# Performance work log

Measured on AMD Instinct MI355X. Metric: run time of the kernel, lower is better.

## Reference

```python
import jax, jax.numpy as jnp
import numpy as np

DILATIONS = (1, 2, 4, 8, 16, 32, 64, 128, 256, 512)
K = 3            # kernel_size
CH = 128         # channels
B, T = 4, 16384
L = len(DILATIONS)


def _conv1x1(x, w, b=None):
    # x: [B, Cin, T], w: [Cout, Cin, 1] -> [B, Cout, T]
    y = jnp.einsum('oc,bct->bot', w[..., 0], x)
    return y if b is None else y + b[None, :, None]


def _causal_dilated_conv(x, w, b, d):
    # buffer of zeros of size (K-1)*d concatenated on the left == causal left pad
    pad = (K - 1) * d
    y = jax.lax.conv_general_dilated(
        x, w, window_strides=(1,), padding=[(pad, 0)], rhs_dilation=(d,),
        dimension_numbers=('NCH', 'OIH', 'NCH'))
    return y + b[None, :, None]


def setup_inputs() -> dict:
    key = jax.random.key(0)
    ks = jax.random.split(key, 12)
    s = 0.1  # keep gated activations out of saturation
    return {
        'x': jax.random.normal(ks[0], (B, 1, T), jnp.float32),
        'c': jax.random.normal(ks[1], (B, 1, T), jnp.float32),
        'head_init': jnp.zeros((B, CH, T), jnp.float32),
        'w_re': jax.random.normal(ks[2], (CH, 1, 1), jnp.float32) * s,
        'conv_w': jax.random.normal(ks[3], (L, 2 * CH, CH, K), jnp.float32) * s,
        'conv_b': jax.random.normal(ks[4], (L, 2 * CH), jnp.float32) * s,
        'mix_w': jax.random.normal(ks[5], (L, 2 * CH, 1, 1), jnp.float32) * s,
        'w1x1': jax.random.normal(ks[6], (L, CH, CH, 1), jnp.float32) * s,
        'b1x1': jax.random.normal(ks[7], (L, CH), jnp.float32) * s,
        'w_head': jax.random.normal(ks[8], (1, CH, 1), jnp.float32) * s,
        'b_head': jax.random.normal(ks[9], (1,), jnp.float32) * s,
    }


def reference(x, c, head_init, w_re, conv_w, conv_b, mix_w, w1x1, b1x1, w_head, b_head):
    h = _conv1x1(x, w_re)               # rechannel: [B, CH, T]
    head = head_init                    # head accumulator (zeros == head_input=None)
    for li, d in enumerate(DILATIONS):  # fixed small layer loop (structurally distinct dilations)
        z = _causal_dilated_conv(h, conv_w[li], conv_b[li], d)   # [B, 2CH, T]
        z = z + _conv1x1(c, mix_w[li])                           # conditioning mixer
        post = jnp.tanh(z[:, :CH]) * jax.nn.sigmoid(z[:, CH:])   # gated activation
        h = h + _conv1x1(post, w1x1[li], b1x1[li])               # residual
        head = head + post
    out = _conv1x1(head, w_head, b_head)  # [B, 1, T]
    return out, h
```

## Files before the change

kernel.cpp:

```cpp
#include <hip/hip_runtime.h>
#include <hip/hip_bf16.h>

#define B_   4
#define T_   16384
#define CH_  128
#define TCH_ 256
#define NL_  10
#define TT_  64
#define SHW_ 196

typedef __attribute__((ext_vector_type(8))) short short8;
typedef __attribute__((ext_vector_type(4))) float f32x4;

#define MFMA16(a, b, c) __builtin_amdgcn_mfma_f32_16x16x32_bf16(a, b, c, 0, 0, 0)

__device__ __forceinline__ unsigned short f2bf(float f) {
  unsigned u = __float_as_uint(f);
  return (unsigned short)((u + 0x7FFFu + ((u >> 16) & 1u)) >> 16);
}
__device__ __forceinline__ float bf2f(unsigned s) {
  return __uint_as_float((s & 0xFFFFu) << 16);
}
__device__ __forceinline__ float fast_tanh(float x) {
  float e = __expf(2.0f * fabsf(x));
  float t = 1.0f - 2.0f / (e + 1.0f);
  return copysignf(t, x);
}
__device__ __forceinline__ float fast_sig(float x) {
  return 1.0f / (1.0f + __expf(-x));
}

__global__ __launch_bounds__(256) void pack_w(
    const float* __restrict__ conv_w, const float* __restrict__ w1x1,
    unsigned short* __restrict__ wpackA, unsigned short* __restrict__ wpack1) {
  const int NA = NL_ * 4 * 4 * 12 * 64 * 8;
  int idx = blockIdx.x * 256 + threadIdx.x;
  if (idx < NA) {
    int j = idx & 7;
    int t1 = idx >> 3;
    int l = t1 & 63;
    int t2 = t1 >> 6;
    int ks = t2 % 12;
    int t3 = t2 / 12;
    int f = t3 & 3;
    int t4 = t3 >> 2;
    int w = t4 & 3;
    int li = t4 >> 2;
    int o = 32 * w + 16 * (f & 1) + 128 * (f >> 1) + (l & 15);
    int ck = 32 * ks + 8 * (l >> 4) + j;
    int c = ck & 127, k = ck >> 7;
    wpackA[idx] = f2bf(conv_w[((li * TCH_ + o) * CH_ + c) * 3 + k]);
  } else {
    int i2 = idx - NA;
    if (i2 < NL_ * 4 * 2 * 4 * 64 * 8) {
      int j = i2 & 7;
      int t1 = i2 >> 3;
      int l = t1 & 63;
      int t2 = t1 >> 6;
      int ks = t2 & 3;
      int t3 = t2 >> 2;
      int p = t3 & 1;
      int t4 = t3 >> 1;
      int w = t4 & 3;
      int li = t4 >> 2;
      int o = 32 * w + 16 * p + (l & 15);
      int c = 32 * ks + 8 * (l >> 4) + j;
      wpack1[i2] = f2bf(w1x1[(li * CH_ + o) * CH_ + c]);
    }
  }
}

__global__ __launch_bounds__(256) void rechannel_k(
    const float* __restrict__ x, const float* __restrict__ w_re,
    unsigned short* __restrict__ hb) {
  int flat = blockIdx.x * 256 + threadIdx.x;
  int cid = flat & 15;
  int t = (flat >> 4) & (T_ - 1);
  int b = flat >> 18;
  float xv = x[b * T_ + t];
  const float* wr = w_re + cid * 8;
  union { short8 s; unsigned short u[8]; } o;
#pragma unroll
  for (int j = 0; j < 8; ++j) o.u[j] = f2bf(wr[j] * xv);
  *(short8*)(hb + (size_t)(b * T_ + t) * CH_ + cid * 8) = o.s;
}

__global__ __launch_bounds__(256) void out_init_k(
    const float* __restrict__ head_init, const float* __restrict__ w_head,
    const float* __restrict__ b_head, float* __restrict__ out) {
  int idx = blockIdx.x * 256 + threadIdx.x;
  int b = idx / T_;
  int t = idx - b * T_;
  float acc = b_head[0];
#pragma unroll 8
  for (int c = 0; c < CH_; ++c)
    acc += w_head[c] * head_init[(b * CH_ + c) * T_ + t];
  out[idx] = acc;
}

__global__ __launch_bounds__(256, 3) void layer_k(
    const unsigned short* __restrict__ hin,
    unsigned short* __restrict__ hob,
    float* __restrict__ hof,
    const float* __restrict__ cin, float* __restrict__ out,
    const unsigned short* __restrict__ wA,
    const unsigned short* __restrict__ w1p,
    const float* __restrict__ bconv,
    const float* __restrict__ wmix,
    const float* __restrict__ b1,
    const float* __restrict__ w_head,
    int d, int is_final) {
  __shared__ unsigned shH[TT_ * SHW_];
  __shared__ float shR[4 * 4 * 16];

  const int tid = threadIdx.x;
  const int b = blockIdx.y;
  const int t0 = blockIdx.x * TT_;

#pragma unroll
  for (int it = 0; it < 12; ++it) {
    int flat = it * 256 + tid;
    int cid = flat & 15;
    int tt = (flat >> 4) & 63;
    int k = flat >> 10;
    int t = t0 + tt - (2 - k) * d;
    uint4 v = make_uint4(0u, 0u, 0u, 0u);
    if (t >= 0)
      v = *(const uint4*)(hin + ((size_t)(b * T_ + t) * CH_ + cid * 8));
    *(uint4*)(shH + tt * SHW_ + k * 64 + cid * 4) = v;
  }
  __syncthreads();

  const int wave = __builtin_amdgcn_readfirstlane(tid >> 6);
  const int lane = tid & 63;
  const int r = lane & 15;
  const int g = lane >> 4;

  f32x4 accL[2][4], accH[2][4];
#pragma unroll
  for (int p = 0; p < 2; ++p)
#pragma unroll
    for (int q = 0; q < 4; ++q) {
      accL[p][q] = (f32x4){0.f, 0.f, 0.f, 0.f};
      accH[p][q] = (f32x4){0.f, 0.f, 0.f, 0.f};
    }

  const short8* wAv = (const short8*)wA;
#pragma unroll
  for (int ks = 0; ks < 12; ++ks) {
    short8 bf[4];
#pragma unroll
    for (int q = 0; q < 4; ++q)
      bf[q] = *(const short8*)(shH + (16 * q + r) * SHW_ + 16 * ks + 4 * g);
    short8 a0 = wAv[((wave * 4 + 0) * 12 + ks) * 64 + lane];
    short8 a1 = wAv[((wave * 4 + 1) * 12 + ks) * 64 + lane];
    short8 a2 = wAv[((wave * 4 + 2) * 12 + ks) * 64 + lane];
    short8 a3 = wAv[((wave * 4 + 3) * 12 + ks) * 64 + lane];
#pragma unroll
    for (int q = 0; q < 4; ++q) {
      accL[0][q] = MFMA16(a0, bf[q], accL[0][q]);
      accL[1][q] = MFMA16(a1, bf[q], accL[1][q]);
      accH[0][q] = MFMA16(a2, bf[q], accH[0][q]);
      accH[1][q] = MFMA16(a3, bf[q], accH[1][q]);
    }
  }
  __syncthreads();

  float cq[4];
#pragma unroll
  for (int q = 0; q < 4; ++q) cq[q] = cin[b * T_ + t0 + 16 * q + r];

  float hs[4] = {0.f, 0.f, 0.f, 0.f};
#pragma unroll
  for (int p = 0; p < 2; ++p) {
    float bcL[4], bcH[4], wmL[4], wmH[4], whv[4];
#pragma unroll
    for (int j = 0; j < 4; ++j) {
      int o = 32 * wave + 16 * p + 4 * g + j;
      bcL[j] = bconv[o];
      bcH[j] = bconv[o + CH_];
      wmL[j] = wmix[o];
      wmH[j] = wmix[o + CH_];
      whv[j] = w_head[o];
    }
#pragma unroll
    for (int q = 0; q < 4; ++q) {
      float pv[4];
#pragma unroll
      for (int j = 0; j < 4; ++j) {
        float zl = accL[p][q][j] + bcL[j] + wmL[j] * cq[q];
        float zh = accH[p][q][j] + bcH[j] + wmH[j] * cq[q];
        pv[j] = fast_tanh(zl) * fast_sig(zh);
        hs[q] += whv[j] * pv[j];
      }
      uint2 pk;
      pk.x = (unsigned)f2bf(pv[0]) | ((unsigned)f2bf(pv[1]) << 16);
      pk.y = (unsigned)f2bf(pv[2]) | ((unsigned)f2bf(pv[3]) << 16);
      *(uint2*)(shH + (16 * q + r) * SHW_ + 16 * wave + 8 * p + 2 * g) = pk;
    }
  }
  __syncthreads();

  f32x4 acc2[2][4];
#pragma unroll
  for (int p = 0; p < 2; ++p)
#pragma unroll
    for (int q = 0; q < 4; ++q) acc2[p][q] = (f32x4){0.f, 0.f, 0.f, 0.f};

  const short8* w1v = (const short8*)w1p;
#pragma unroll
  for (int ks = 0; ks < 4; ++ks) {
    short8 bp[4];
#pragma unroll
    for (int q = 0; q < 4; ++q)
      bp[q] = *(const short8*)(shH + (16 * q + r) * SHW_ + 16 * ks + 4 * g);
    short8 a0 = w1v[((wave * 2 + 0) * 4 + ks) * 64 + lane];
    short8 a1 = w1v[((wave * 2 + 1) * 4 + ks) * 64 + lane];
#pragma unroll
    for (int q = 0; q < 4; ++q) {
      acc2[0][q] = MFMA16(a0, bp[q], acc2[0][q]);
      acc2[1][q] = MFMA16(a1, bp[q], acc2[1][q]);
    }
  }

  float res[2][4][4];
  const int o0b = 32 * wave + 4 * g;
#pragma unroll
  for (int p = 0; p < 2; ++p) {
    const int o0 = o0b + 16 * p;
    float b1v[4];
#pragma unroll
    for (int j = 0; j < 4; ++j) b1v[j] = b1[o0 + j];
#pragma unroll
    for (int q = 0; q < 4; ++q) {
      uint2 hv = *(const uint2*)(shH + (16 * q + r) * SHW_ + 128 + (o0 >> 1));
      res[p][q][0] = bf2f(hv.x) + b1v[0] + acc2[p][q][0];
      res[p][q][1] = bf2f(hv.x >> 16) + b1v[1] + acc2[p][q][1];
      res[p][q][2] = bf2f(hv.y) + b1v[2] + acc2[p][q][2];
      res[p][q][3] = bf2f(hv.y >> 16) + b1v[3] + acc2[p][q][3];
    }
  }

#pragma unroll
  for (int q = 0; q < 4; ++q) {
    hs[q] += __shfl_xor(hs[q], 16);
    hs[q] += __shfl_xor(hs[q], 32);
  }
  if (g == 0) {
#pragma unroll
    for (int q = 0; q < 4; ++q) shR[(wave * 4 + q) * 16 + r] = hs[q];
  }
  __syncthreads();

  if (tid < 64) {
    int q = tid >> 4, rr = tid & 15;
    float tot = shR[(0 * 4 + q) * 16 + rr] + shR[(1 * 4 + q) * 16 + rr] +
                shR[(2 * 4 + q) * 16 + rr] + shR[(3 * 4 + q) * 16 + rr];
    out[b * T_ + t0 + 16 * q + rr] += tot;
  }

  if (!is_final) {
#pragma unroll
    for (int p = 0; p < 2; ++p) {
      const int o0 = o0b + 16 * p;
#pragma unroll
      for (int q = 0; q < 4; ++q) {
        uint2 pk;
        pk.x = (unsigned)f2bf(res[p][q][0]) | ((unsigned)f2bf(res[p][q][1]) << 16);
        pk.y = (unsigned)f2bf(res[p][q][2]) | ((unsigned)f2bf(res[p][q][3]) << 16);
        *(uint2*)(shH + (16 * q + r) * SHW_ + (o0 >> 1)) = pk;
      }
    }
    __syncthreads();
#pragma unroll
    for (int it = 0; it < 4; ++it) {
      int flat = it * 256 + tid;
      int cid = flat & 15;
      int tt = flat >> 4;
      *(uint4*)(hob + ((size_t)(b * T_ + t0 + tt) * CH_ + cid * 8)) =
          *(const uint4*)(shH + tt * SHW_ + cid * 4);
    }
  } else {
#pragma unroll
    for (int p = 0; p < 2; ++p) {
      const int o0 = o0b + 16 * p;
#pragma unroll
      for (int q = 0; q < 4; ++q) {
#pragma unroll
        for (int j = 0; j < 4; ++j)
          hof[(size_t)(b * CH_ + o0 + j) * T_ + t0 + 16 * q + r] = res[p][q][j];
      }
    }
  }
}

extern "C" void kernel_launch(void* const* d_in, const int* in_sizes, int n_in,
                              void* d_out, int out_size, void* d_ws, size_t ws_size,
                              hipStream_t stream) {
  const float* x         = (const float*)d_in[0];
  const float* c         = (const float*)d_in[1];
  const float* head_init = (const float*)d_in[2];
  const float* w_re      = (const float*)d_in[3];
  const float* conv_w    = (const float*)d_in[4];
  const float* conv_b    = (const float*)d_in[5];
  const float* mix_w     = (const float*)d_in[6];
  const float* w1x1      = (const float*)d_in[7];
  const float* b1x1      = (const float*)d_in[8];
  const float* w_head    = (const float*)d_in[9];
  const float* b_head    = (const float*)d_in[10];

  float* out = (float*)d_out;
  float* hof = out + B_ * T_;

  unsigned short* hb0 = (unsigned short*)d_ws;
  unsigned short* hb1 = hb0 + (size_t)B_ * T_ * CH_;
  unsigned short* wpackA = hb1 + (size_t)B_ * T_ * CH_;
  unsigned short* wpack1 = wpackA + NL_ * 4 * 4 * 12 * 64 * 8;

  const int n_pack = NL_ * 4 * 4 * 12 * 64 * 8 + NL_ * 4 * 2 * 4 * 64 * 8;
  pack_w<<<(n_pack + 255) / 256, 256, 0, stream>>>(conv_w, w1x1, wpackA, wpack1);

  rechannel_k<<<(B_ * T_ * 16) / 256, 256, 0, stream>>>(x, w_re, hb0);
  out_init_k<<<(B_ * T_) / 256, 256, 0, stream>>>(head_init, w_head, b_head, out);

  const int dil[NL_] = {1, 2, 4, 8, 16, 32, 64, 128, 256, 512};
  for (int li = 0; li < NL_; ++li) {
    const unsigned short* hin = (li & 1) ? hb1 : hb0;
    unsigned short* hob       = (li & 1) ? hb0 : hb1;
    int is_final = (li == NL_ - 1);
    layer_k<<<dim3(T_ / TT_, B_), 256, 0, stream>>>(
        hin, hob, hof, c, out,
        wpackA + li * (4 * 4 * 12 * 64 * 8),
        wpack1 + li * (4 * 2 * 4 * 64 * 8),
        conv_b + li * TCH_,
        mix_w + li * TCH_,
        b1x1 + li * CH_,
        w_head,
        dil[li], is_final);
  }
}
```

Before: 333.1 us.

## Fuse layer launches into one persistent kernel with per-tile dataflow flags

Replaces the ten per-layer launches with a single persistent kernel of 512 blocks, each handling two time tiles across all layers. Tiles wait on release/acquire flags from the producer tiles of the previous layer that their dilated window needs, instead of on a full kernel boundary. Each layer writes to its own h buffer, which removes write-after-read hazards, and the head output is accumulated in registers rather than read and written in global memory every layer. The cost is spin-waiting, a larger workspace, and a risk of deadlock if the 512 blocks cannot all be resident at once. Tile ordering can also serialise work, since tile g1 of a layer runs only after g0.

Measured after the change: 841.6 us. +152.6%, slower.

```diff
diff --git a/kernel.cpp b/kernel.cpp
--- a/kernel.cpp
+++ b/kernel.cpp
@@ -8,6 +8,8 @@
 #define NL_  10
 #define TT_  64
 #define SHW_ 196
+#define HSZ_ (B_ * T_ * CH_)
+#define NBLK_ 512
 
 typedef __attribute__((ext_vector_type(8))) short short8;
 typedef __attribute__((ext_vector_type(4))) float f32x4;
@@ -98,24 +100,33 @@
   out[idx] = acc;
 }
 
-__global__ __launch_bounds__(256, 3) void layer_k(
+__device__ __forceinline__ void layer_tile(
+    int li, int d, int g,
     const unsigned short* __restrict__ hin,
-    unsigned short* __restrict__ hob,
+    unsigned short* __restrict__ hout,
     float* __restrict__ hof,
-    const float* __restrict__ cin, float* __restrict__ out,
+    const float* __restrict__ cin,
     const unsigned short* __restrict__ wA,
     const unsigned short* __restrict__ w1p,
-    const float* __restrict__ bconv,
-    const float* __restrict__ wmix,
-    const float* __restrict__ b1,
-    const float* __restrict__ w_head,
-    int d, int is_final) {
-  __shared__ unsigned shH[TT_ * SHW_];
-  __shared__ float shR[4 * 4 * 16];
-
-  const int tid = threadIdx.x;
-  const int b = blockIdx.y;
-  const int t0 = blockIdx.x * TT_;
+    const float* __restrict__ bconv, const float* __restrict__ wmix,
+    const float* __restrict__ b1, const float* __restrict__ w_head,
+    int* __restrict__ flags, float& outAcc,
+    unsigned* shH, float* shR, int tid) {
+  const int b = g >> 8;
+  const int n = g & 255;
+  const int t0 = n * TT_;
+
+  if (li > 0) {
+    int nb = (2 * d + 63) >> 6;
+    if (nb > n) nb = n;
+    if (tid <= nb) {
+      int* fp = flags + (li - 1) * 1024 + (g - tid);
+      while (__hip_atomic_load(fp, __ATOMIC_ACQUIRE,
+                               __HIP_MEMORY_SCOPE_AGENT) == 0)
+        __builtin_amdgcn_s_sleep(2);
+    }
+  }
+  __syncthreads();
 
 #pragma unroll
   for (int it = 0; it < 12; ++it) {
@@ -134,7 +145,7 @@
   const int wave = __builtin_amdgcn_readfirstlane(tid >> 6);
   const int lane = tid & 63;
   const int r = lane & 15;
-  const int g = lane >> 4;
+  const int gg = lane >> 4;
 
   f32x4 accL[2][4], accH[2][4];
 #pragma unroll
@@ -151,7 +162,7 @@
     short8 bf[4];
 #pragma unroll
     for (int q = 0; q < 4; ++q)
-      bf[q] = *(const short8*)(shH + (16 * q + r) * SHW_ + 16 * ks + 4 * g);
+      bf[q] = *(const short8*)(shH + (16 * q + r) * SHW_ + 16 * ks + 4 * gg);
     short8 a0 = wAv[((wave * 4 + 0) * 12 + ks) * 64 + lane];
     short8 a1 = wAv[((wave * 4 + 1) * 12 + ks) * 64 + lane];
     short8 a2 = wAv[((wave * 4 + 2) * 12 + ks) * 64 + lane];
@@ -176,7 +187,7 @@
     float bcL[4], bcH[4], wmL[4], wmH[4], whv[4];
 #pragma unroll
     for (int j = 0; j < 4; ++j) {
-      int o = 32 * wave + 16 * p + 4 * g + j;
+      int o = 32 * wave + 16 * p + 4 * gg + j;
       bcL[j] = bconv[o];
       bcH[j] = bconv[o + CH_];
       wmL[j] = wmix[o];
@@ -196,7 +207,7 @@
       uint2 pk;
       pk.x = (unsigned)f2bf(pv[0]) | ((unsigned)f2bf(pv[1]) << 16);
       pk.y = (unsigned)f2bf(pv[2]) | ((unsigned)f2bf(pv[3]) << 16);
-      *(uint2*)(shH + (16 * q + r) * SHW_ + 16 * wave + 8 * p + 2 * g) = pk;
+      *(uint2*)(shH + (16 * q + r) * SHW_ + 16 * wave + 8 * p + 2 * gg) = pk;
     }
   }
   __syncthreads();
@@ -213,7 +224,7 @@
     short8 bp[4];
 #pragma unroll
     for (int q = 0; q < 4; ++q)
-      bp[q] = *(const short8*)(shH + (16 * q + r) * SHW_ + 16 * ks + 4 * g);
+      bp[q] = *(const short8*)(shH + (16 * q + r) * SHW_ + 16 * ks + 4 * gg);
     short8 a0 = w1v[((wave * 2 + 0) * 4 + ks) * 64 + lane];
     short8 a1 = w1v[((wave * 2 + 1) * 4 + ks) * 64 + lane];
 #pragma unroll
@@ -224,7 +235,7 @@
   }
 
   float res[2][4][4];
-  const int o0b = 32 * wave + 4 * g;
+  const int o0b = 32 * wave + 4 * gg;
 #pragma unroll
   for (int p = 0; p < 2; ++p) {
     const int o0 = o0b + 16 * p;
@@ -246,7 +257,7 @@
     hs[q] += __shfl_xor(hs[q], 16);
     hs[q] += __shfl_xor(hs[q], 32);
   }
-  if (g == 0) {
+  if (gg == 0) {
 #pragma unroll
     for (int q = 0; q < 4; ++q) shR[(wave * 4 + q) * 16 + r] = hs[q];
   }
@@ -254,12 +265,11 @@
 
   if (tid < 64) {
     int q = tid >> 4, rr = tid & 15;
-    float tot = shR[(0 * 4 + q) * 16 + rr] + shR[(1 * 4 + q) * 16 + rr] +
-                shR[(2 * 4 + q) * 16 + rr] + shR[(3 * 4 + q) * 16 + rr];
-    out[b * T_ + t0 + 16 * q + rr] += tot;
-  }
-
-  if (!is_final) {
+    outAcc += shR[(0 * 4 + q) * 16 + rr] + shR[(1 * 4 + q) * 16 + rr] +
+              shR[(2 * 4 + q) * 16 + rr] + shR[(3 * 4 + q) * 16 + rr];
+  }
+
+  if (li < NL_ - 1) {
 #pragma unroll
     for (int p = 0; p < 2; ++p) {
       const int o0 = o0b + 16 * p;
@@ -277,9 +287,13 @@
       int flat = it * 256 + tid;
       int cid = flat & 15;
       int tt = flat >> 4;
-      *(uint4*)(hob + ((size_t)(b * T_ + t0 + tt) * CH_ + cid * 8)) =
+      *(uint4*)(hout + ((size_t)(b * T_ + t0 + tt) * CH_ + cid * 8)) =
           *(const uint4*)(shH + tt * SHW_ + cid * 4);
     }
+    __syncthreads();
+    if (tid == 0)
+      __hip_atomic_store(flags + li * 1024 + g, 1, __ATOMIC_RELEASE,
+                         __HIP_MEMORY_SCOPE_AGENT);
   } else {
 #pragma unroll
     for (int p = 0; p < 2; ++p) {
@@ -291,6 +305,53 @@
           hof[(size_t)(b * CH_ + o0 + j) * T_ + t0 + 16 * q + r] = res[p][q][j];
       }
     }
+  }
+}
+
+__global__ __launch_bounds__(256, 3) void stack_k(
+    unsigned short* __restrict__ hbase,
+    float* __restrict__ hof,
+    const float* __restrict__ cin, float* __restrict__ out,
+    const unsigned short* __restrict__ wpackA,
+    const unsigned short* __restrict__ wpack1,
+    const float* __restrict__ conv_b, const float* __restrict__ mix_w,
+    const float* __restrict__ b1x1, const float* __restrict__ w_head,
+    int* __restrict__ flags) {
+  __shared__ unsigned shH[TT_ * SHW_];
+  __shared__ float shR[4 * 4 * 16];
+
+  const int tid = threadIdx.x;
+  const int g0 = blockIdx.x;
+  const int g1 = blockIdx.x + NBLK_;
+
+  float outAcc0 = 0.f, outAcc1 = 0.f;
+  if (tid < 64) {
+    int q = tid >> 4, rr = tid & 15;
+    outAcc0 = out[(g0 >> 8) * T_ + (g0 & 255) * TT_ + 16 * q + rr];
+    outAcc1 = out[(g1 >> 8) * T_ + (g1 & 255) * TT_ + 16 * q + rr];
+  }
+
+#pragma unroll 1
+  for (int li = 0; li < NL_; ++li) {
+    const int d = 1 << li;
+    const unsigned short* hin = hbase + (size_t)li * HSZ_;
+    unsigned short* hout = hbase + (size_t)(li + 1) * HSZ_;
+    const unsigned short* wA  = wpackA + li * (4 * 4 * 12 * 64 * 8);
+    const unsigned short* w1p = wpack1 + li * (4 * 2 * 4 * 64 * 8);
+    const float* bconv = conv_b + li * TCH_;
+    const float* wmix  = mix_w + li * TCH_;
+    const float* b1    = b1x1 + li * CH_;
+
+    layer_tile(li, d, g0, hin, hout, hof, cin, wA, w1p, bconv, wmix, b1,
+               w_head, flags, outAcc0, shH, shR, tid);
+    layer_tile(li, d, g1, hin, hout, hof, cin, wA, w1p, bconv, wmix, b1,
+               w_head, flags, outAcc1, shH, shR, tid);
+  }
+
+  if (tid < 64) {
+    int q = tid >> 4, rr = tid & 15;
+    out[(g0 >> 8) * T_ + (g0 & 255) * TT_ + 16 * q + rr] = outAcc0;
+    out[(g1 >> 8) * T_ + (g1 & 255) * TT_ + 16 * q + rr] = outAcc1;
   }
 }
 
@@ -312,30 +373,20 @@
   float* out = (float*)d_out;
   float* hof = out + B_ * T_;
 
-  unsigned short* hb0 = (unsigned short*)d_ws;
-  unsigned short* hb1 = hb0 + (size_t)B_ * T_ * CH_;
-  unsigned short* wpackA = hb1 + (size_t)B_ * T_ * CH_;
+  unsigned short* hbase  = (unsigned short*)d_ws;
+  unsigned short* wpackA = hbase + (size_t)11 * HSZ_;
   unsigned short* wpack1 = wpackA + NL_ * 4 * 4 * 12 * 64 * 8;
+  int* flags = (int*)(wpack1 + NL_ * 4 * 2 * 4 * 64 * 8);
+
+  hipMemsetAsync(flags, 0, 9 * 1024 * sizeof(int), stream);
 
   const int n_pack = NL_ * 4 * 4 * 12 * 64 * 8 + NL_ * 4 * 2 * 4 * 64 * 8;
   pack_w<<<(n_pack + 255) / 256, 256, 0, stream>>>(conv_w, w1x1, wpackA, wpack1);
 
-  rechannel_k<<<(B_ * T_ * 16) / 256, 256, 0, stream>>>(x, w_re, hb0);
+  rechannel_k<<<(B_ * T_ * 16) / 256, 256, 0, stream>>>(x, w_re, hbase);
   out_init_k<<<(B_ * T_) / 256, 256, 0, stream>>>(head_init, w_head, b_head, out);
 
-  const int dil[NL_] = {1, 2, 4, 8, 16, 32, 64, 128, 256, 512};
-  for (int li = 0; li < NL_; ++li) {
-    const unsigned short* hin = (li & 1) ? hb1 : hb0;
-    unsigned short* hob       = (li & 1) ? hb0 : hb1;
-    int is_final = (li == NL_ - 1);
-    layer_k<<<dim3(T_ / TT_, B_), 256, 0, stream>>>(
-        hin, hob, hof, c, out,
-        wpackA + li * (4 * 4 * 12 * 64 * 8),
-        wpack1 + li * (4 * 2 * 4 * 64 * 8),
-        conv_b + li * TCH_,
-        mix_w + li * TCH_,
-        b1x1 + li * CH_,
-        w_head,
-        dil[li], is_final);
-  }
-}
+  stack_k<<<NBLK_, 256, 0, stream>>>(hbase, hof, c, out, wpackA, wpack1,
+                                     conv_b, mix_w, b1x1, w_head,
+                                     (int*)flags);
+}
```
